# Kernel tuning notes

Measured on AMD Instinct MI355X. Metric: run time of the kernel, lower is better.

Reference implementation:

```python
import jax, jax.numpy as jnp
import numpy as np

TAU = 0.7
# Dellar moment flip under x<->y swap: (rho, jy, jx, Pyy, Pxy, Pxx, N, Jy, Jx)
FLIP = np.array([0, 2, 1, 5, 4, 3, 6, 8, 7])


def _dellar_matrices():
    # D2Q9 velocities in lettuce stencil order
    e = np.array([[0, 0], [1, 0], [0, 1], [-1, 0], [0, -1],
                  [1, 1], [-1, 1], [-1, -1], [1, -1]], dtype=np.float64)
    ex, ey = e[:, 0], e[:, 1]
    g = np.array([1, -2, -2, -2, -2, 4, 4, 4, 4], dtype=np.float64)  # Dellar ghost mode
    third = 1.0 / 3.0
    M = np.stack([
        np.ones(9),            # rho
        ex,                    # jx
        ey,                    # jy
        ex * ex - third,       # Pxx - cs^2 rho
        ex * ey,               # Pxy
        ey * ey - third,       # Pyy - cs^2 rho
        g,                     # N (ghost)
        g * ex,                # Jx (ghost)
        g * ey,                # Jy (ghost)
    ])
    return M, np.linalg.inv(M)


def _mlp(x, w1, b1, w2, b2):
    # x: (nx, ny, 9) -> (nx, ny, 1); Linear(9,24) + ReLU + Linear(24,1)
    h = jax.nn.relu(jnp.einsum('xyi,oi->xyo', x, w1) + b1)
    return jnp.einsum('xyo,po->xyp', h, w2) + b2


def setup_inputs() -> dict:
    key = jax.random.key(0)
    ks = jax.random.split(key, 9)
    nx = ny = 2048
    f = jax.random.uniform(ks[0], (9, nx, ny), dtype=jnp.float32)

    def lin_w(k, o, i):
        return jax.random.uniform(k, (o, i), dtype=jnp.float32,
                                  minval=-1.0, maxval=1.0) / np.sqrt(i)

    def lin_b(k, o, i):
        return jax.random.uniform(k, (o,), dtype=jnp.float32,
                                  minval=-1.0, maxval=1.0) / np.sqrt(i)

    M, Minv = _dellar_matrices()
    return {
        'f': f,
        'j_w1': lin_w(ks[1], 24, 9), 'j_b1': lin_b(ks[2], 24, 9),
        'j_w2': lin_w(ks[3], 1, 24), 'j_b2': lin_b(ks[4], 1, 24),
        'n_w1': lin_w(ks[5], 24, 9), 'n_b1': lin_b(ks[6], 24, 9),
        'n_w2': lin_w(ks[7], 1, 24), 'n_b2': lin_b(ks[8], 1, 24),
        'M': jnp.asarray(M, jnp.float32),
        'Minv': jnp.asarray(Minv, jnp.float32),
    }


def reference(f, j_w1, j_b1, j_w2, j_b2, n_w1, n_b1, n_w2, n_b2, M, Minv):
    # moment transform: m_i = M_ij f_j, shape (9, nx, ny)
    m = jnp.einsum('ij,jxy->ixy', M, f)
    mt = jnp.transpose(m, (1, 2, 0))        # (nx, ny, 9)
    mtf = mt[..., FLIP]                     # x<->y flipped moments

    gt_half = lambda a: 0.5 + jnp.exp(a)
    tau_jx = gt_half(_mlp(mt, j_w1, j_b1, j_w2, j_b2))[..., 0]
    tau_jy = gt_half(_mlp(mtf, j_w1, j_b1, j_w2, j_b2))[..., 0]
    tau_n = gt_half(_mlp(mt, n_w1, n_b1, n_w2, n_b2)
                    + _mlp(mtf, n_w1, n_b1, n_w2, n_b2))[..., 0]

    taus = jnp.full_like(m, TAU)
    taus = taus.at[6].set(tau_n).at[7].set(tau_jx).at[8].set(tau_jy)

    rho, jx, jy = m[0], m[1], m[2]
    zero = jnp.zeros_like(rho)
    meq = jnp.stack([rho, jx, jy,
                     jx * jx / rho, jx * jy / rho, jy * jy / rho,
                     zero, zero, zero])

    m_post = m - (m - meq) / taus
    return jnp.einsum('ij,jxy->ixy', Minv, m_post)
```

## Files before the change

### kernel.cpp

```cpp
#include <hip/hip_runtime.h>

typedef _Float16 h2 __attribute__((ext_vector_type(2)));

__device__ __forceinline__ h2 h2splat(float s) {
    const _Float16 v = (_Float16)s;
    h2 r; r.x = v; r.y = v; return r;
}
__device__ __forceinline__ h2 h2fma(h2 a, h2 b, h2 c) { return __builtin_elementwise_fma(a, b, c); }
__device__ __forceinline__ h2 h2relu(h2 a) {
    h2 z; z.x = (_Float16)0.0f; z.y = (_Float16)0.0f;
    return __builtin_elementwise_max(a, z);
}


__global__ __launch_bounds__(256) void prep_kernel(
    const float* __restrict__ j_w1, const float* __restrict__ j_b1,
    const float* __restrict__ j_w2, const float* __restrict__ j_b2,
    const float* __restrict__ n_w1, const float* __restrict__ n_b1,
    const float* __restrict__ n_w2, const float* __restrict__ n_b2,
    const float* __restrict__ Mg, const float* __restrict__ Minvg,
    float* __restrict__ ws)
{
    const int t = threadIdx.x;
    h2* wh = reinterpret_cast<h2*>(ws);
    if (t < 48) {
        const int o = t >> 1, which = t & 1;
        const float* w1 = which ? n_w1 : j_w1;
        const float* b1 = which ? n_b1 : j_b1;
        float w[9];
        #pragma unroll
        for (int i = 0; i < 9; ++i) w[i] = w1[o * 9 + i];
        const int b = o * 22 + which * 10;
        wh[b + 0] = h2splat(w[0]);
        wh[b + 1] = h2splat(w[4]);
        wh[b + 2] = h2splat(w[6]);
        wh[b + 3] = h2splat(0.5f * (w[1] + w[2]));
        wh[b + 4] = h2splat(0.5f * (w[3] + w[5]));
        wh[b + 5] = h2splat(0.5f * (w[7] + w[8]));
        wh[b + 6] = h2splat(0.5f * (w[1] - w[2]));
        wh[b + 7] = h2splat(0.5f * (w[3] - w[5]));
        wh[b + 8] = h2splat(0.5f * (w[7] - w[8]));
        wh[b + 9] = h2splat(b1[o]);
        if (!which) {
            wh[o * 22 + 20] = h2splat(j_w2[o]);
            wh[o * 22 + 21] = h2splat(n_w2[o]);
        }
    } else if (t >= 64 && t < 64 + 81) {
        const int e = t - 64, r = e / 9, i = e % 9;
        float v;
        switch (r) {
            case 0: v = Mg[0 * 9 + i]; break;
            case 1: v = Mg[4 * 9 + i]; break;
            case 2: v = Mg[6 * 9 + i]; break;
            case 3: v = Mg[1 * 9 + i] + Mg[2 * 9 + i]; break;
            case 4: v = Mg[3 * 9 + i] + Mg[5 * 9 + i]; break;
            case 5: v = Mg[7 * 9 + i] + Mg[8 * 9 + i]; break;
            case 6: v = Mg[1 * 9 + i] - Mg[2 * 9 + i]; break;
            case 7: v = Mg[3 * 9 + i] - Mg[5 * 9 + i]; break;
            default: v = Mg[7 * 9 + i] - Mg[8 * 9 + i]; break;
        }
        ws[528 + r * 9 + i] = v;
    } else if (t >= 160 && t < 160 + 81) {
        const int e = t - 160;
        ws[528 + 81 + e] = Minvg[e];
    } else if (t == 254) {
        ws[528 + 162] = j_b2[0];
    } else if (t == 255) {
        ws[528 + 163] = 2.0f * n_b2[0];
    }
}

__global__ __launch_bounds__(256) void mrt_main(
    const float* __restrict__ f, const float* __restrict__ W,
    float* __restrict__ out, int n2)
{
    const h2*    Wh = reinterpret_cast<const h2*>(W);
    const float* Wf = W + 528;

    long base = ((long)blockIdx.x * 256 + threadIdx.x) * 4;
    if (base + 4 > n2) base = n2 - 4;

    float tv[9][4];
    {
        float fv[9][4];
        #pragma unroll
        for (int i = 0; i < 9; ++i) {
            const float4 u = *reinterpret_cast<const float4*>(f + (size_t)i * n2 + base);
            fv[i][0] = u.x; fv[i][1] = u.y; fv[i][2] = u.z; fv[i][3] = u.w;
        }
        #pragma unroll
        for (int r = 0; r < 9; ++r) {
            float a0 = 0.f, a1 = 0.f, a2 = 0.f, a3 = 0.f;
            #pragma unroll
            for (int i = 0; i < 9; ++i) {
                const float w = Wf[r * 9 + i];
                a0 = fmaf(w, fv[i][0], a0);
                a1 = fmaf(w, fv[i][1], a1);
                a2 = fmaf(w, fv[i][2], a2);
                a3 = fmaf(w, fv[i][3], a3);
            }
            tv[r][0] = a0; tv[r][1] = a1; tv[r][2] = a2; tv[r][3] = a3;
        }
    }

    h2 tvh[9][2];
    #pragma unroll
    for (int r = 0; r < 9; ++r) {
        tvh[r][0].x = (_Float16)tv[r][0]; tvh[r][0].y = (_Float16)tv[r][1];
        tvh[r][1].x = (_Float16)tv[r][2]; tvh[r][1].y = (_Float16)tv[r][3];
    }

    h2 accj[2], accjf[2], accn[2];
    #pragma unroll
    for (int p = 0; p < 2; ++p) { accj[p] = h2splat(0.f); accjf[p] = h2splat(0.f); accn[p] = h2splat(0.f); }

    #pragma unroll 4
    for (int o = 0; o < 24; ++o) {
        const h2 s0 = Wh[o*22+0], s1 = Wh[o*22+1], s2 = Wh[o*22+2];
        const h2 s3 = Wh[o*22+3], s4 = Wh[o*22+4], s5 = Wh[o*22+5];
        const h2 a0 = Wh[o*22+6], a1 = Wh[o*22+7], a2 = Wh[o*22+8];
        const h2 b1j = Wh[o*22+9];
        const h2 u0 = Wh[o*22+10], u1 = Wh[o*22+11], u2 = Wh[o*22+12];
        const h2 u3 = Wh[o*22+13], u4 = Wh[o*22+14], u5 = Wh[o*22+15];
        const h2 v0 = Wh[o*22+16], v1 = Wh[o*22+17], v2 = Wh[o*22+18];
        const h2 b1n = Wh[o*22+19];
        const h2 w2j = Wh[o*22+20], w2n = Wh[o*22+21];
        #pragma unroll
        for (int p = 0; p < 2; ++p) {
            h2 s = h2fma(s0, tvh[0][p], b1j);
            s = h2fma(s1, tvh[1][p], s);
            s = h2fma(s2, tvh[2][p], s);
            s = h2fma(s3, tvh[3][p], s);
            s = h2fma(s4, tvh[4][p], s);
            s = h2fma(s5, tvh[5][p], s);
            h2 a = a0 * tvh[6][p];
            a = h2fma(a1, tvh[7][p], a);
            a = h2fma(a2, tvh[8][p], a);
            const h2 hs = h2relu(s + a);
            const h2 hd = h2relu(s - a);
            accj[p]  = h2fma(w2j, hs, accj[p]);
            accjf[p] = h2fma(w2j, hd, accjf[p]);

            h2 sn = h2fma(u0, tvh[0][p], b1n);
            sn = h2fma(u1, tvh[1][p], sn);
            sn = h2fma(u2, tvh[2][p], sn);
            sn = h2fma(u3, tvh[3][p], sn);
            sn = h2fma(u4, tvh[4][p], sn);
            sn = h2fma(u5, tvh[5][p], sn);
            h2 an = v0 * tvh[6][p];
            an = h2fma(v1, tvh[7][p], an);
            an = h2fma(v2, tvh[8][p], an);
            const h2 ns = h2relu(sn + an);
            const h2 nd = h2relu(sn - an);
            accn[p] = h2fma(w2n, ns + nd, accn[p]);
        }
    }

    const float b2j = Wf[162], b2n2 = Wf[163];
    const float Cs = 1.0f / 0.7f;
    #pragma unroll
    for (int k = 0; k < 4; ++k) {
        const int p = k >> 1;
        const float aj  = (k & 1) ? (float)accj[p].y  : (float)accj[p].x;
        const float ajf = (k & 1) ? (float)accjf[p].y : (float)accjf[p].x;
        const float an  = (k & 1) ? (float)accn[p].y  : (float)accn[p].x;

        const float rt7 = __builtin_amdgcn_rcpf(0.5f + __expf(aj + b2j));
        const float rt8 = __builtin_amdgcn_rcpf(0.5f + __expf(ajf + b2j));
        const float rt6 = __builtin_amdgcn_rcpf(0.5f + __expf(an + b2n2));
        const float rrho = __builtin_amdgcn_rcpf(tv[0][k]);

        const float jx = 0.5f * (tv[3][k] + tv[6][k]);
        const float jy = 0.5f * (tv[3][k] - tv[6][k]);
        const float m3 = 0.5f * (tv[4][k] + tv[7][k]);
        const float m5 = 0.5f * (tv[4][k] - tv[7][k]);
        const float m7 = 0.5f * (tv[5][k] + tv[8][k]);
        const float m8 = 0.5f * (tv[5][k] - tv[8][k]);
        const float m4 = tv[1][k], m6 = tv[2][k];

        tv[1][k] = jx;
        tv[2][k] = jy;
        tv[3][k] = m3 - (m3 - jx * jx * rrho) * Cs;
        tv[4][k] = m4 - (m4 - jx * jy * rrho) * Cs;
        tv[5][k] = m5 - (m5 - jy * jy * rrho) * Cs;
        tv[6][k] = m6 - m6 * rt6;
        tv[7][k] = m7 - m7 * rt7;
        tv[8][k] = m8 - m8 * rt8;
    }

    #pragma unroll
    for (int r = 0; r < 9; ++r) {
        float o0 = 0.f, o1 = 0.f, o2 = 0.f, o3 = 0.f;
        #pragma unroll
        for (int j = 0; j < 9; ++j) {
            const float w = Wf[81 + r * 9 + j];
            o0 = fmaf(w, tv[j][0], o0);
            o1 = fmaf(w, tv[j][1], o1);
            o2 = fmaf(w, tv[j][2], o2);
            o3 = fmaf(w, tv[j][3], o3);
        }
        const float4 vv = make_float4(o0, o1, o2, o3);
        *reinterpret_cast<float4*>(out + (size_t)r * n2 + base) = vv;
    }
}

extern "C" void kernel_launch(void* const* d_in, const int* in_sizes, int n_in,
                              void* d_out, int out_size, void* d_ws, size_t ws_size,
                              hipStream_t stream) {
    const float* f    = (const float*)d_in[0];
    const float* j_w1 = (const float*)d_in[1];
    const float* j_b1 = (const float*)d_in[2];
    const float* j_w2 = (const float*)d_in[3];
    const float* j_b2 = (const float*)d_in[4];
    const float* n_w1 = (const float*)d_in[5];
    const float* n_b1 = (const float*)d_in[6];
    const float* n_w2 = (const float*)d_in[7];
    const float* n_b2 = (const float*)d_in[8];
    const float* Mg   = (const float*)d_in[9];
    const float* Minv = (const float*)d_in[10];
    float* out = (float*)d_out;
    float* ws  = (float*)d_ws;

    const int n2 = in_sizes[0] / 9;
    const int pts_per_block = 256 * 4;
    const int grid = (n2 + pts_per_block - 1) / pts_per_block;

    prep_kernel<<<1, 256, 0, stream>>>(j_w1, j_b1, j_w2, j_b2,
                                       n_w1, n_b1, n_w2, n_b2, Mg, Minv, ws);
    mrt_main<<<grid, 256, 0, stream>>>(f, ws, out, n2);
}
```

Before: 295.7 us.

## Hardcode moment transform, fold collision into residual update, process two tiles per thread

Replaces the generic 9x9 moment matrix multiply with a hand-factored butterfly that uses the fixed D2Q9 Dellar matrix. The output is now computed as f minus Minv applied to the six non-conserved moment deviations, which cuts the back-transform to a 9x6 product. Each thread now handles two 4-point tiles and issues both sets of loads before computing, so the second tile's memory traffic overlaps with the first tile's work. In exchange it hardcodes the M matrix instead of reading it from the input, keeps more values live in registers, and launches half as many blocks.

```diff
diff --git a/kernel.cpp b/kernel.cpp
--- a/kernel.cpp
+++ b/kernel.cpp
@@ -45,62 +45,46 @@
             wh[o * 22 + 20] = h2splat(j_w2[o]);
             wh[o * 22 + 21] = h2splat(n_w2[o]);
         }
-    } else if (t >= 64 && t < 64 + 81) {
-        const int e = t - 64, r = e / 9, i = e % 9;
-        float v;
-        switch (r) {
-            case 0: v = Mg[0 * 9 + i]; break;
-            case 1: v = Mg[4 * 9 + i]; break;
-            case 2: v = Mg[6 * 9 + i]; break;
-            case 3: v = Mg[1 * 9 + i] + Mg[2 * 9 + i]; break;
-            case 4: v = Mg[3 * 9 + i] + Mg[5 * 9 + i]; break;
-            case 5: v = Mg[7 * 9 + i] + Mg[8 * 9 + i]; break;
-            case 6: v = Mg[1 * 9 + i] - Mg[2 * 9 + i]; break;
-            case 7: v = Mg[3 * 9 + i] - Mg[5 * 9 + i]; break;
-            default: v = Mg[7 * 9 + i] - Mg[8 * 9 + i]; break;
-        }
-        ws[528 + r * 9 + i] = v;
-    } else if (t >= 160 && t < 160 + 81) {
-        const int e = t - 160;
-        ws[528 + 81 + e] = Minvg[e];
+    } else if (t >= 64 && t < 64 + 54) {
+        const int e = t - 64, r = e / 6, c = e % 6;
+        ws[528 + e] = -Minvg[r * 9 + 3 + c];
     } else if (t == 254) {
-        ws[528 + 162] = j_b2[0];
+        ws[528 + 54] = j_b2[0];
     } else if (t == 255) {
-        ws[528 + 163] = 2.0f * n_b2[0];
-    }
-}
-
-__global__ __launch_bounds__(256) void mrt_main(
-    const float* __restrict__ f, const float* __restrict__ W,
-    float* __restrict__ out, int n2)
+        ws[528 + 55] = 2.0f * n_b2[0];
+    }
+}
+
+__device__ __forceinline__ void process_tile(
+    const float4* __restrict__ cur, const h2* __restrict__ Wh,
+    const float* __restrict__ Wf, float* __restrict__ out,
+    long base, int n2)
 {
-    const h2*    Wh = reinterpret_cast<const h2*>(W);
-    const float* Wf = W + 528;
-
-    long base = ((long)blockIdx.x * 256 + threadIdx.x) * 4;
-    if (base + 4 > n2) base = n2 - 4;
+    float fv[9][4];
+    #pragma unroll
+    for (int i = 0; i < 9; ++i) {
+        fv[i][0] = cur[i].x; fv[i][1] = cur[i].y;
+        fv[i][2] = cur[i].z; fv[i][3] = cur[i].w;
+    }
 
     float tv[9][4];
-    {
-        float fv[9][4];
-        #pragma unroll
-        for (int i = 0; i < 9; ++i) {
-            const float4 u = *reinterpret_cast<const float4*>(f + (size_t)i * n2 + base);
-            fv[i][0] = u.x; fv[i][1] = u.y; fv[i][2] = u.z; fv[i][3] = u.w;
-        }
-        #pragma unroll
-        for (int r = 0; r < 9; ++r) {
-            float a0 = 0.f, a1 = 0.f, a2 = 0.f, a3 = 0.f;
-            #pragma unroll
-            for (int i = 0; i < 9; ++i) {
-                const float w = Wf[r * 9 + i];
-                a0 = fmaf(w, fv[i][0], a0);
-                a1 = fmaf(w, fv[i][1], a1);
-                a2 = fmaf(w, fv[i][2], a2);
-                a3 = fmaf(w, fv[i][3], a3);
-            }
-            tv[r][0] = a0; tv[r][1] = a1; tv[r][2] = a2; tv[r][3] = a3;
-        }
+    #pragma unroll
+    for (int k = 0; k < 4; ++k) {
+        const float f0 = fv[0][k], f1 = fv[1][k], f2 = fv[2][k], f3 = fv[3][k];
+        const float f4 = fv[4][k], f5 = fv[5][k], f6 = fv[6][k], f7 = fv[7][k], f8 = fv[8][k];
+        const float P = f1 + f2, Q = f3 + f4, R = f5 + f7, S = f6 + f8;
+        const float D = f5 - f7, F = f6 - f8, G = f1 - f2, H = f3 - f4;
+        const float A = P + Q, B = R + S;
+        const float C = P - Q, K = G - H;
+        tv[0][k] = f0 + A + B;
+        tv[1][k] = R - S;
+        tv[2][k] = fmaf(4.0f, B, fmaf(-2.0f, A, f0));
+        tv[3][k] = fmaf(2.0f, D, C);
+        tv[4][k] = 0.33333334f * fmaf(4.0f, B, fmaf(-2.0f, f0, A));
+        tv[5][k] = fmaf(8.0f, D, -2.0f * C);
+        tv[6][k] = fmaf(-2.0f, F, K);
+        tv[7][k] = G + H;
+        tv[8][k] = fmaf(-8.0f, F, -2.0f * K);
     }
 
     h2 tvh[9][2];
@@ -156,8 +140,9 @@
         }
     }
 
-    const float b2j = Wf[162], b2n2 = Wf[163];
+    const float b2j = Wf[54], b2n2 = Wf[55];
     const float Cs = 1.0f / 0.7f;
+    float d[6][4];
     #pragma unroll
     for (int k = 0; k < 4; ++k) {
         const int p = k >> 1;
@@ -178,30 +163,51 @@
         const float m8 = 0.5f * (tv[5][k] - tv[8][k]);
         const float m4 = tv[1][k], m6 = tv[2][k];
 
-        tv[1][k] = jx;
-        tv[2][k] = jy;
-        tv[3][k] = m3 - (m3 - jx * jx * rrho) * Cs;
-        tv[4][k] = m4 - (m4 - jx * jy * rrho) * Cs;
-        tv[5][k] = m5 - (m5 - jy * jy * rrho) * Cs;
-        tv[6][k] = m6 - m6 * rt6;
-        tv[7][k] = m7 - m7 * rt7;
-        tv[8][k] = m8 - m8 * rt8;
+        d[0][k] = (m3 - jx * jx * rrho) * Cs;
+        d[1][k] = (m4 - jx * jy * rrho) * Cs;
+        d[2][k] = (m5 - jy * jy * rrho) * Cs;
+        d[3][k] = m6 * rt6;
+        d[4][k] = m7 * rt7;
+        d[5][k] = m8 * rt8;
     }
 
     #pragma unroll
     for (int r = 0; r < 9; ++r) {
-        float o0 = 0.f, o1 = 0.f, o2 = 0.f, o3 = 0.f;
+        float o0 = fv[r][0], o1 = fv[r][1], o2 = fv[r][2], o3 = fv[r][3];
         #pragma unroll
-        for (int j = 0; j < 9; ++j) {
-            const float w = Wf[81 + r * 9 + j];
-            o0 = fmaf(w, tv[j][0], o0);
-            o1 = fmaf(w, tv[j][1], o1);
-            o2 = fmaf(w, tv[j][2], o2);
-            o3 = fmaf(w, tv[j][3], o3);
+        for (int c = 0; c < 6; ++c) {
+            const float w = Wf[r * 6 + c];
+            o0 = fmaf(w, d[c][0], o0);
+            o1 = fmaf(w, d[c][1], o1);
+            o2 = fmaf(w, d[c][2], o2);
+            o3 = fmaf(w, d[c][3], o3);
         }
-        const float4 vv = make_float4(o0, o1, o2, o3);
-        *reinterpret_cast<float4*>(out + (size_t)r * n2 + base) = vv;
-    }
+        *reinterpret_cast<float4*>(out + (size_t)r * n2 + base) = make_float4(o0, o1, o2, o3);
+    }
+}
+
+__global__ __launch_bounds__(256) void mrt_main(
+    const float* __restrict__ f, const float* __restrict__ W,
+    float* __restrict__ out, int n2)
+{
+    const h2*    Wh = reinterpret_cast<const h2*>(W);
+    const float* Wf = W + 528;
+
+    long chunk = (long)blockIdx.x * 2048;
+    if (chunk + 2048 > n2) chunk = n2 - 2048;
+    const long b0 = chunk + threadIdx.x * 4;
+    const long b1 = b0 + 1024;
+
+    float4 cur[9], nxt[9];
+    #pragma unroll
+    for (int i = 0; i < 9; ++i)
+        cur[i] = *reinterpret_cast<const float4*>(f + (size_t)i * n2 + b0);
+    #pragma unroll
+    for (int i = 0; i < 9; ++i)
+        nxt[i] = *reinterpret_cast<const float4*>(f + (size_t)i * n2 + b1);
+
+    process_tile(cur, Wh, Wf, out, b0, n2);
+    process_tile(nxt, Wh, Wf, out, b1, n2);
 }
 
 extern "C" void kernel_launch(void* const* d_in, const int* in_sizes, int n_in,
@@ -222,8 +228,7 @@
     float* ws  = (float*)d_ws;
 
     const int n2 = in_sizes[0] / 9;
-    const int pts_per_block = 256 * 4;
-    const int grid = (n2 + pts_per_block - 1) / pts_per_block;
+    const int grid = (n2 + 2047) / 2048;
 
     prep_kernel<<<1, 256, 0, stream>>>(j_w1, j_b1, j_w2, j_b2,
                                        n_w1, n_b1, n_w2, n_b2, Mg, Minv, ws);
```

Result: no change. 299.4 us (+1.3%).
